# Kernel tuning notes

Measured on AMD Instinct MI355X. Metric: run time of the kernel, lower is better.

The kernel has to match this reference:

```python
import jax, jax.numpy as jnp
import numpy as np

B, T, H, W, C = 8, 16, 64, 64, 16
HID = 64  # hidden_dim of each ConvLSTM cell
K = 3     # kernel size


def _convlstm_step(x, h, c, Wk, b):
    # conv over concat([x, h]) -> 4*HID gate channels (i, f, o, g)
    z = jax.lax.conv_general_dilated(
        jnp.concatenate([x, h], axis=-1), Wk,
        window_strides=(1, 1), padding='SAME',
        dimension_numbers=('NHWC', 'HWIO', 'NHWC')) + b
    i, f, o, g = jnp.split(z, 4, axis=-1)
    c_new = jax.nn.sigmoid(f) * c + jax.nn.sigmoid(i) * jnp.tanh(g)
    h_new = jax.nn.sigmoid(o) * jnp.tanh(c_new)
    return h_new, c_new


def setup_inputs() -> dict:
    key = jax.random.key(0)
    k1, k2, k3 = jax.random.split(key, 3)
    enc_input = jax.random.normal(k1, (B, T, H, W, C), jnp.float32)
    # input cell: in_channels = C + HID; stacked hidden cell: 2*HID
    W0 = jax.random.normal(k2, (K, K, C + HID, 4 * HID), jnp.float32) * 0.05
    b0 = jnp.zeros((4 * HID,), jnp.float32)
    W1 = jax.random.normal(k3, (K, K, 2 * HID, 4 * HID), jnp.float32) * 0.05
    b1 = jnp.zeros((4 * HID,), jnp.float32)
    return {"enc_input": enc_input, "W0": W0, "b0": b0, "W1": W1, "b1": b1}


def reference(enc_input, W0, b0, W1, b1):
    Bv, Tv, Hv, Wv, _ = enc_input.shape
    z0 = jnp.zeros((Bv, Hv, Wv, HID), enc_input.dtype)

    def step(carry, x_t):
        h0, c0, h1, c1 = carry
        h0, c0 = _convlstm_step(x_t, h0, c0, W0, b0)   # input ConvLSTM
        h1, c1 = _convlstm_step(h0, h1, c1, W1, b1)    # stacked hidden ConvLSTM
        return (h0, c0, h1, c1), None

    xs = jnp.moveaxis(enc_input, 1, 0)  # [T, B, H, W, C]
    (h0, c0, h1, c1), _ = jax.lax.scan(step, (z0, z0, z0, z0), xs)
    # Encoder returns last hidden layer's (h, c)
    return (h1, c1)
```

## Files before the change

kernel.cpp:

```cpp
#include <hip/hip_runtime.h>
#include <hip/hip_bf16.h>

#define Bv 8
#define Tv 16
#define Hv 64
#define Wv 64
#define Cv 16
#define HID 64
#define PH 66

typedef short short8 __attribute__((ext_vector_type(8)));
typedef float f32x4 __attribute__((ext_vector_type(4)));
typedef unsigned short u16x8 __attribute__((ext_vector_type(8)));

__device__ __forceinline__ unsigned short f2bf(float x) {
  union { float f; unsigned int u; } v; v.f = x;
  unsigned int r = v.u + 0x7FFF + ((v.u >> 16) & 1);
  return (unsigned short)(r >> 16);
}
__device__ __forceinline__ float sigmoid_f(float x) {
  return 1.f / (1.f + __expf(-x));
}
__device__ __forceinline__ float tanh_f(float x) {
  float e = __expf(2.f * x);
  return 1.f - 2.f / (e + 1.f);
}

__global__ void relayout_w0(const float* __restrict__ W0, unsigned short* __restrict__ out) {
  int o = blockIdx.x * 256 + threadIdx.x;
  if (o >= 27 * 8192) return;
  int cc = o >> 13, t = o & 8191;
  int wn = t >> 11, t2 = t & 2047;
  int g = t2 >> 9, t3 = t2 & 511;
  int l = t3 >> 3, e = t3 & 7;
  int kg = l >> 4, r = l & 15;
  int k = kg * 8 + e;
  int col = g * 64 + wn * 16 + r;
  int tap = cc / 3, cgi = cc - tap * 3;
  int p = cgi * 32 + k;
  float v = 0.f;
  if (p < 16)        v = W0[(size_t)(tap * 80 + p) * 256 + col];
  else if (p >= 32)  v = W0[(size_t)(tap * 80 + (p - 16)) * 256 + col];
  out[o] = f2bf(v);
}
__global__ void relayout_w1(const float* __restrict__ W1, unsigned short* __restrict__ out) {
  int o = blockIdx.x * 256 + threadIdx.x;
  if (o >= 36 * 8192) return;
  int cc = o >> 13, t = o & 8191;
  int wn = t >> 11, t2 = t & 2047;
  int g = t2 >> 9, t3 = t2 & 511;
  int l = t3 >> 3, e = t3 & 7;
  int kg = l >> 4, r = l & 15;
  int k = kg * 8 + e;
  int col = g * 64 + wn * 16 + r;
  int tap = cc >> 2, cgi = cc & 3;
  out[o] = f2bf(W1[(size_t)(tap * 128 + cgi * 32 + k) * 256 + col]);
}

__global__ void zero_init(unsigned short* __restrict__ h0a, unsigned short* __restrict__ h0b,
                          unsigned short* __restrict__ h1a, unsigned short* __restrict__ h1b,
                          unsigned short* __restrict__ xb) {
  int idx = blockIdx.x * 256 + threadIdx.x;
  u16x8 z = {};
  const int XB_CH = (Bv * PH * PH * 32 * 2) / 16;
  if (idx < XB_CH) { *(u16x8*)(xb + idx * 8) = z; return; }
  idx -= XB_CH;
  int bufi = idx / 16640;
  if (bufi >= 4) return;
  int rem = idx - bufi * 16640;
  int b = rem / 2080, r2 = rem - b * 2080;
  int hp = r2 >> 3, c8 = r2 & 7;
  int y, x;
  if (hp < 66)       { y = 0;  x = hp; }
  else if (hp < 132) { y = 65; x = hp - 66; }
  else { int i2 = hp - 132; y = 1 + (i2 >> 1); x = (i2 & 1) * 65; }
  unsigned short* base = (bufi == 0) ? h0a : (bufi == 1) ? h0b : (bufi == 2) ? h1a : h1b;
  *(u16x8*)(base + ((size_t)((b * PH + y) * PH) + x) * 64 + c8 * 8) = z;
}

__global__ void convert_x0(const float* __restrict__ enc, unsigned short* __restrict__ xb) {
  int idx = blockIdx.x * 256 + threadIdx.x;
  int b = idx >> 12, pix = idx & 4095;
  int y = pix >> 6, x = pix & 63;
  const float* s = enc + ((size_t)(b * Tv + 0) * 4096 + pix) * 16;
  float4 f0 = *(const float4*)(s);
  float4 f1 = *(const float4*)(s + 4);
  float4 f2 = *(const float4*)(s + 8);
  float4 f3 = *(const float4*)(s + 12);
  u16x8 o0, o1;
  o0[0]=f2bf(f0.x); o0[1]=f2bf(f0.y); o0[2]=f2bf(f0.z); o0[3]=f2bf(f0.w);
  o0[4]=f2bf(f1.x); o0[5]=f2bf(f1.y); o0[6]=f2bf(f1.z); o0[7]=f2bf(f1.w);
  o1[0]=f2bf(f2.x); o1[1]=f2bf(f2.y); o1[2]=f2bf(f2.z); o1[3]=f2bf(f2.w);
  o1[4]=f2bf(f3.x); o1[5]=f2bf(f3.y); o1[6]=f2bf(f3.z); o1[7]=f2bf(f3.w);
  unsigned short* d = xb + ((size_t)((b * PH + y + 1) * PH) + (x + 1)) * 32;
  *(u16x8*)(d)     = o0;
  *(u16x8*)(d + 8) = o1;
}

template<int CELL, bool T0>
__global__ __launch_bounds__(512, 2)
void cell_mfma(const unsigned short* __restrict__ A0, const unsigned short* __restrict__ A1,
               const unsigned short* __restrict__ Wr, const float* __restrict__ bias,
               float* __restrict__ cbuf, unsigned short* __restrict__ hout,
               float* __restrict__ h1f, float* __restrict__ c1f,
               const float* __restrict__ enc, int tnext, unsigned short* __restrict__ xnext)
{
  constexpr int NC = T0 ? (CELL == 0 ? 9 : 18) : (CELL == 0 ? 27 : 36);
  extern __shared__ char lds[];

  const int tid = threadIdx.x;
  const int l = tid & 63, w = tid >> 6;
  const int wm = w >> 2, wn = w & 3;
  const int gid = blockIdx.x;
  const int bx = gid & 7, by = (gid >> 3) & 3, b = gid >> 5;
  const int r = l & 15, kg = l >> 4;
  const int j = wn * 16 + r;

  const char* bases[2] = {(const char*)A0, (const char*)A1};

  int pixs;
  {
    int ps = w * 16 + r;
    int ys = by * 16 + (ps >> 3), xs = bx * 8 + (ps & 7);
    pixs = (b * PH + ys) * PH + xs;
  }

  float bi[4];
#pragma unroll
  for (int g = 0; g < 4; ++g) bi[g] = bias[g * 64 + j];
  float cpre[4][4] = {};
  if constexpr (!T0) {
#pragma unroll
    for (int mi = 0; mi < 4; ++mi) {
#pragma unroll
      for (int rg = 0; rg < 4; ++rg) {
        int p = wm * 64 + mi * 16 + kg * 4 + rg;
        int y = by * 16 + (p >> 3), x = bx * 8 + (p & 7);
        cpre[mi][rg] = cbuf[((size_t)((b * Hv + y) * Wv) + x) * HID + j];
      }
    }
  }

  auto ISSUE = [&](int cc, int buf) {
    char* dst = lds + buf * 24576;
    int tap, cgi, wcc;
    if (CELL == 0) {
      if (T0) { tap = cc; cgi = 0; wcc = cc * 3; }
      else    { tap = cc / 3; cgi = cc - tap * 3; wcc = cc; }
    } else {
      if (T0) { tap = cc >> 1; cgi = cc & 1; wcc = tap * 4 + cgi; }
      else    { tap = cc >> 2; cgi = cc & 3; wcc = cc; }
    }
    int ky = tap / 3, kx = tap - ky * 3;
    const char* srcb;
    unsigned aoff;
    if (CELL == 0) {
      if (cgi == 0) { srcb = bases[0]; aoff = (unsigned)((pixs + ky * PH + kx) * 64 + kg * 16); }
      else { srcb = bases[1];
             aoff = (unsigned)((pixs + ky * PH + kx) * 128 + ((cgi == 2) ? 64 : 0) + kg * 16); }
    } else {
      srcb = bases[cgi >> 1];
      aoff = (unsigned)((pixs + ky * PH + kx) * 128 + (cgi & 1) * 64 + kg * 16);
    }
    __builtin_amdgcn_global_load_lds((const unsigned int*)(srcb + aoff),
                                     (unsigned int*)(dst + w * 1024), 16, 0, 0);
    const char* wp = (const char*)Wr + (size_t)wcc * 16384 + (unsigned)(w * 2048 + l * 16);
    __builtin_amdgcn_global_load_lds((const unsigned int*)(wp),
                                     (unsigned int*)(dst + 8192 + w * 2048), 16, 0, 0);
    __builtin_amdgcn_global_load_lds((const unsigned int*)(wp + 1024),
                                     (unsigned int*)(dst + 8192 + w * 2048 + 1024), 16, 0, 0);
  };

  f32x4 acc[4][4] = {};
  short8 af[2][4], bfv[2][4];

  ISSUE(0, 0); ISSUE(1, 1); ISSUE(2, 2); ISSUE(3, 3);
#pragma unroll
  for (int cc = 0; cc < NC; ++cc) {
    if (cc <= NC - 4)      { asm volatile("s_waitcnt vmcnt(9)" ::: "memory"); }
    else if (cc == NC - 3) { asm volatile("s_waitcnt vmcnt(6)" ::: "memory"); }
    else if (cc == NC - 2) { asm volatile("s_waitcnt vmcnt(3)" ::: "memory"); }
    else                   { asm volatile("s_waitcnt vmcnt(0)" ::: "memory"); }
    __builtin_amdgcn_sched_barrier(0);
    __builtin_amdgcn_s_barrier();
    __builtin_amdgcn_sched_barrier(0);

    const int q = cc & 1;
    const char* bufp = lds + (cc % 5) * 24576;
#pragma unroll
    for (int mi = 0; mi < 4; ++mi)
      af[q][mi] = *(const short8*)(bufp + (wm * 4 + mi) * 1024 + l * 16);
#pragma unroll
    for (int g = 0; g < 4; ++g)
      bfv[q][g] = *(const short8*)(bufp + 8192 + (wn * 4 + g) * 1024 + l * 16);

    if (cc > 0) {
      asm volatile("s_waitcnt lgkmcnt(8)" ::: "memory");
      __builtin_amdgcn_sched_barrier(0);
    }
    if (cc + 4 < NC) ISSUE(cc + 4, (cc + 4) % 5);
    if (cc > 0) {
      const int qp = q ^ 1;
#pragma unroll
      for (int mi = 0; mi < 4; ++mi)
#pragma unroll
        for (int g = 0; g < 4; ++g)
          acc[mi][g] = __builtin_amdgcn_mfma_f32_16x16x32_bf16(
              af[qp][mi], bfv[qp][g], acc[mi][g], 0, 0, 0);
    }
  }
  asm volatile("s_waitcnt lgkmcnt(0)" ::: "memory");
  __builtin_amdgcn_sched_barrier(0);
  {
    const int qp = (NC - 1) & 1;
#pragma unroll
    for (int mi = 0; mi < 4; ++mi)
#pragma unroll
      for (int g = 0; g < 4; ++g)
        acc[mi][g] = __builtin_amdgcn_mfma_f32_16x16x32_bf16(
            af[qp][mi], bfv[qp][g], acc[mi][g], 0, 0, 0);
  }

#pragma unroll
  for (int mi = 0; mi < 4; ++mi) {
#pragma unroll
    for (int rg = 0; rg < 4; ++rg) {
      int p = wm * 64 + mi * 16 + kg * 4 + rg;
      int y = by * 16 + (p >> 3), x = bx * 8 + (p & 7);
      float zi = acc[mi][0][rg] + bi[0];
      float zf = acc[mi][1][rg] + bi[1];
      float zo = acc[mi][2][rg] + bi[2];
      float zg = acc[mi][3][rg] + bi[3];
      float co = cpre[mi][rg];
      float cn = sigmoid_f(zf) * co + sigmoid_f(zi) * tanh_f(zg);
      float hn = sigmoid_f(zo) * tanh_f(cn);
      size_t ci = ((size_t)((b * Hv + y) * Wv) + x) * HID + j;
      cbuf[ci] = cn;
      hout[((size_t)((b * PH + y + 1) * PH) + (x + 1)) * HID + j] = f2bf(hn);
      if (CELL == 1 && h1f != nullptr) {
        h1f[ci] = hn;
        c1f[ci] = cn;
      }
    }
  }

  if (CELL == 1 && tnext < Tv) {
    int px = gid * 128 + (tid >> 2), q4 = tid & 3;
    int bb = px >> 12, pix = px & 4095;
    int y = pix >> 6, x = pix & 63;
    const float* s = enc + ((size_t)(bb * Tv + tnext) * 4096 + pix) * 16 + q4 * 4;
    float4 f = *(const float4*)s;
    unsigned short* d = xnext + ((size_t)((bb * PH + y + 1) * PH) + (x + 1)) * 32 + q4 * 4;
    d[0] = f2bf(f.x); d[1] = f2bf(f.y); d[2] = f2bf(f.z); d[3] = f2bf(f.w);
  }
}

extern "C" void kernel_launch(void* const* d_in, const int* in_sizes, int n_in,
                              void* d_out, int out_size, void* d_ws, size_t ws_size,
                              hipStream_t stream) {
  const float* enc = (const float*)d_in[0];
  const float* W0  = (const float*)d_in[1];
  const float* b0  = (const float*)d_in[2];
  const float* W1  = (const float*)d_in[3];
  const float* b1  = (const float*)d_in[4];

  float* out = (float*)d_out;
  const size_t NST = (size_t)Bv * Hv * Wv * HID;
  float* h1f = out;
  float* c1  = out + NST;

  char* ws = (char*)d_ws;
  const size_t SZ_C = NST * 4;
  const size_t SZ_H = (size_t)Bv * PH * PH * HID * 2;
  const size_t SZ_X = (size_t)Bv * PH * PH * 32 * 2;
  float*          c0  = (float*)ws;
  unsigned short* h0a = (unsigned short*)(ws + SZ_C);
  unsigned short* h0b = (unsigned short*)(ws + SZ_C + SZ_H);
  unsigned short* h1a = (unsigned short*)(ws + SZ_C + 2 * SZ_H);
  unsigned short* h1b = (unsigned short*)(ws + SZ_C + 3 * SZ_H);
  unsigned short* xb  = (unsigned short*)(ws + SZ_C + 4 * SZ_H);
  unsigned short* w0r = (unsigned short*)(ws + SZ_C + 4 * SZ_H + SZ_X);
  unsigned short* w1r = (unsigned short*)(ws + SZ_C + 4 * SZ_H + SZ_X + (size_t)27 * 16384);

  hipFuncSetAttribute((const void*)cell_mfma<0,false>, hipFuncAttributeMaxDynamicSharedMemorySize, 131072);
  hipFuncSetAttribute((const void*)cell_mfma<0,true>,  hipFuncAttributeMaxDynamicSharedMemorySize, 131072);
  hipFuncSetAttribute((const void*)cell_mfma<1,false>, hipFuncAttributeMaxDynamicSharedMemorySize, 131072);
  hipFuncSetAttribute((const void*)cell_mfma<1,true>,  hipFuncAttributeMaxDynamicSharedMemorySize, 131072);

  zero_init<<<805, 256, 0, stream>>>(h0a, h0b, h1a, h1b, xb);
  relayout_w0<<<864, 256, 0, stream>>>(W0, w0r);
  relayout_w1<<<1152, 256, 0, stream>>>(W1, w1r);
  convert_x0<<<128, 256, 0, stream>>>(enc, xb);

  dim3 grid(256), block(512);
  for (int t = 0; t < Tv; ++t) {
    const bool last = (t == Tv - 1);
    unsigned short* h0r = (t & 1) ? h0b : h0a;
    unsigned short* h0w = (t & 1) ? h0a : h0b;
    unsigned short* h1r = (t & 1) ? h1b : h1a;
    unsigned short* h1w = (t & 1) ? h1a : h1b;
    if (t == 0) {
      cell_mfma<0,true><<<grid, block, 122880, stream>>>(
          xb, h0r, w0r, b0, c0, h0w, nullptr, nullptr, nullptr, Tv, nullptr);
      cell_mfma<1,true><<<grid, block, 122880, stream>>>(
          h0w, h1r, w1r, b1, c1, h1w, nullptr, nullptr, enc, 1, xb);
    } else {
      cell_mfma<0,false><<<grid, block, 122880, stream>>>(
          xb, h0r, w0r, b0, c0, h0w, nullptr, nullptr, nullptr, Tv, nullptr);
      cell_mfma<1,false><<<grid, block, 122880, stream>>>(
          h0w, h1r, w1r, b1, c1, h1w, last ? h1f : nullptr, last ? c1 : nullptr,
          enc, t + 1, xb);
    }
  }
}
```

Baseline: 714.8 us.

## Load weight fragments directly into registers, shrinking the LDS ring to activations only

Weight B-fragments now go straight from global memory into a 4-deep register ring via inline global_load_dwordx4, two chunks ahead, instead of being staged through LDS. The LDS ring now holds only the activation tiles, which cuts dynamic shared memory from 120 KB to 40 KB per block. This could let two blocks share a CU and removes the LDS reads for weights. In exchange it uses more VGPRs and needs hand-computed vmcnt wait counts that must match the order of the mixed loads exactly.

```diff
diff --git a/kernel.cpp b/kernel.cpp
--- a/kernel.cpp
+++ b/kernel.cpp
@@ -24,6 +24,33 @@
 __device__ __forceinline__ float tanh_f(float x) {
   float e = __expf(2.f * x);
   return 1.f - 2.f / (e + 1.f);
+}
+
+__device__ __forceinline__ void waitv_rt(int n) {
+  if      (n <= 0)  asm volatile("s_waitcnt vmcnt(0)" ::: "memory");
+  else if (n == 1)  asm volatile("s_waitcnt vmcnt(1)" ::: "memory");
+  else if (n == 2)  asm volatile("s_waitcnt vmcnt(2)" ::: "memory");
+  else if (n == 3)  asm volatile("s_waitcnt vmcnt(3)" ::: "memory");
+  else if (n == 4)  asm volatile("s_waitcnt vmcnt(4)" ::: "memory");
+  else if (n == 5)  asm volatile("s_waitcnt vmcnt(5)" ::: "memory");
+  else if (n == 6)  asm volatile("s_waitcnt vmcnt(6)" ::: "memory");
+  else if (n == 7)  asm volatile("s_waitcnt vmcnt(7)" ::: "memory");
+  else if (n == 8)  asm volatile("s_waitcnt vmcnt(8)" ::: "memory");
+  else if (n == 9)  asm volatile("s_waitcnt vmcnt(9)" ::: "memory");
+  else if (n == 10) asm volatile("s_waitcnt vmcnt(10)" ::: "memory");
+  else if (n == 11) asm volatile("s_waitcnt vmcnt(11)" ::: "memory");
+  else              asm volatile("s_waitcnt vmcnt(12)" ::: "memory");
+}
+__device__ __forceinline__ constexpr int bS(int i, int NC) {
+  return ((i + 2 <= NC - 1) ? 4 : 0) + ((i + 4 <= NC - 1) ? 1 : 0);
+}
+__device__ __forceinline__ constexpr int NWAIT(int cc, int NC) {
+  if (cc >= NC - 1) return 0;
+  if (cc == 0) return 11;
+  if (cc == 1) return 9;
+  if (cc == 2) return 10;
+  int n = bS(cc - 3, NC) + bS(cc - 2, NC) + bS(cc - 1, NC) - 4;
+  return n < 0 ? 0 : n;
 }
 
 __global__ void relayout_w0(const float* __restrict__ W0, unsigned short* __restrict__ out) {
@@ -141,15 +168,23 @@
     }
   }
 
-  auto ISSUE = [&](int cc, int buf) {
-    char* dst = lds + buf * 24576;
-    int tap, cgi, wcc;
+  const unsigned long long wbase = (unsigned long long)Wr;
+  const unsigned wvo_base = (unsigned)(wn * 4096 + l * 16);
+
+  auto wcc_of = [&](int cc) -> int {
+    if (CELL == 0) return T0 ? cc * 3 : cc;
+    else           return T0 ? ((cc >> 1) * 4 + (cc & 1)) : cc;
+  };
+
+  auto ISSUE_A = [&](int cc, int buf) {
+    char* dst = lds + buf * 8192;
+    int tap, cgi;
     if (CELL == 0) {
-      if (T0) { tap = cc; cgi = 0; wcc = cc * 3; }
-      else    { tap = cc / 3; cgi = cc - tap * 3; wcc = cc; }
+      if (T0) { tap = cc; cgi = 0; }
+      else    { tap = cc / 3; cgi = cc - tap * 3; }
     } else {
-      if (T0) { tap = cc >> 1; cgi = cc & 1; wcc = tap * 4 + cgi; }
-      else    { tap = cc >> 2; cgi = cc & 3; wcc = cc; }
+      if (T0) { tap = cc >> 1; cgi = cc & 1; }
+      else    { tap = cc >> 2; cgi = cc & 3; }
     }
     int ky = tap / 3, kx = tap - ky * 3;
     const char* srcb;
@@ -164,61 +199,75 @@
     }
     __builtin_amdgcn_global_load_lds((const unsigned int*)(srcb + aoff),
                                      (unsigned int*)(dst + w * 1024), 16, 0, 0);
-    const char* wp = (const char*)Wr + (size_t)wcc * 16384 + (unsigned)(w * 2048 + l * 16);
-    __builtin_amdgcn_global_load_lds((const unsigned int*)(wp),
-                                     (unsigned int*)(dst + 8192 + w * 2048), 16, 0, 0);
-    __builtin_amdgcn_global_load_lds((const unsigned int*)(wp + 1024),
-                                     (unsigned int*)(dst + 8192 + w * 2048 + 1024), 16, 0, 0);
   };
 
+  short8 bfv[4][4];
+
+  auto ISSUE_W = [&](int cc) {
+    const int s = cc & 3;
+    unsigned vo = wvo_base + (unsigned)(wcc_of(cc) * 16384);
+    asm volatile("global_load_dwordx4 %0, %1, %2"
+                 : "=&v"(bfv[s][0]) : "v"(vo), "s"(wbase) : "memory");
+    asm volatile("global_load_dwordx4 %0, %1, %2 offset:1024"
+                 : "=&v"(bfv[s][1]) : "v"(vo), "s"(wbase) : "memory");
+    asm volatile("global_load_dwordx4 %0, %1, %2 offset:2048"
+                 : "=&v"(bfv[s][2]) : "v"(vo), "s"(wbase) : "memory");
+    asm volatile("global_load_dwordx4 %0, %1, %2 offset:3072"
+                 : "=&v"(bfv[s][3]) : "v"(vo), "s"(wbase) : "memory");
+  };
+
   f32x4 acc[4][4] = {};
-  short8 af[2][4], bfv[2][4];
-
-  ISSUE(0, 0); ISSUE(1, 1); ISSUE(2, 2); ISSUE(3, 3);
+  short8 af[2][4];
+
+  ISSUE_A(0, 0); __builtin_amdgcn_sched_barrier(0);
+  ISSUE_A(1, 1); __builtin_amdgcn_sched_barrier(0);
+  ISSUE_A(2, 2); __builtin_amdgcn_sched_barrier(0);
+  ISSUE_A(3, 3); __builtin_amdgcn_sched_barrier(0);
+  ISSUE_W(0);    __builtin_amdgcn_sched_barrier(0);
+  ISSUE_W(1);    __builtin_amdgcn_sched_barrier(0);
+
 #pragma unroll
   for (int cc = 0; cc < NC; ++cc) {
-    if (cc <= NC - 4)      { asm volatile("s_waitcnt vmcnt(9)" ::: "memory"); }
-    else if (cc == NC - 3) { asm volatile("s_waitcnt vmcnt(6)" ::: "memory"); }
-    else if (cc == NC - 2) { asm volatile("s_waitcnt vmcnt(3)" ::: "memory"); }
-    else                   { asm volatile("s_waitcnt vmcnt(0)" ::: "memory"); }
+    waitv_rt(NWAIT(cc, NC));
     __builtin_amdgcn_sched_barrier(0);
     __builtin_amdgcn_s_barrier();
     __builtin_amdgcn_sched_barrier(0);
 
     const int q = cc & 1;
-    const char* bufp = lds + (cc % 5) * 24576;
+    const char* bufp = lds + (cc % 5) * 8192;
 #pragma unroll
     for (int mi = 0; mi < 4; ++mi)
       af[q][mi] = *(const short8*)(bufp + (wm * 4 + mi) * 1024 + l * 16);
-#pragma unroll
-    for (int g = 0; g < 4; ++g)
-      bfv[q][g] = *(const short8*)(bufp + 8192 + (wn * 4 + g) * 1024 + l * 16);
 
     if (cc > 0) {
-      asm volatile("s_waitcnt lgkmcnt(8)" ::: "memory");
+      asm volatile("s_waitcnt lgkmcnt(4)" ::: "memory");
       __builtin_amdgcn_sched_barrier(0);
     }
-    if (cc + 4 < NC) ISSUE(cc + 4, (cc + 4) % 5);
+    if (cc + 2 < NC) ISSUE_W(cc + 2);
+    __builtin_amdgcn_sched_barrier(0);
+    if (cc + 4 < NC) ISSUE_A(cc + 4, (cc + 4) % 5);
+    __builtin_amdgcn_sched_barrier(0);
+
     if (cc > 0) {
-      const int qp = q ^ 1;
+      const int qp = (cc - 1) & 1, sp = (cc - 1) & 3;
 #pragma unroll
       for (int mi = 0; mi < 4; ++mi)
 #pragma unroll
         for (int g = 0; g < 4; ++g)
           acc[mi][g] = __builtin_amdgcn_mfma_f32_16x16x32_bf16(
-              af[qp][mi], bfv[qp][g], acc[mi][g], 0, 0, 0);
+              af[qp][mi], bfv[sp][g], acc[mi][g], 0, 0, 0);
     }
   }
   asm volatile("s_waitcnt lgkmcnt(0)" ::: "memory");
   __builtin_amdgcn_sched_barrier(0);
   {
-    const int qp = (NC - 1) & 1;
+    const int qp = (NC - 1) & 1, sp = (NC - 1) & 3;
 #pragma unroll
     for (int mi = 0; mi < 4; ++mi)
 #pragma unroll
       for (int g = 0; g < 4; ++g)
         acc[mi][g] = __builtin_amdgcn_mfma_f32_16x16x32_bf16(
-            af[qp][mi], bfv[qp][g], acc[mi][g], 0, 0, 0);
+            af[qp][mi], bfv[sp][g], acc[mi][g], 0, 0, 0);
   }
 
 #pragma unroll
@@ -282,10 +331,10 @@
   unsigned short* w0r = (unsigned short*)(ws + SZ_C + 4 * SZ_H + SZ_X);
   unsigned short* w1r = (unsigned short*)(ws + SZ_C + 4 * SZ_H + SZ_X + (size_t)27 * 16384);
 
-  hipFuncSetAttribute((const void*)cell_mfma<0,false>, hipFuncAttributeMaxDynamicSharedMemorySize, 131072);
-  hipFuncSetAttribute((const void*)cell_mfma<0,true>,  hipFuncAttributeMaxDynamicSharedMemorySize, 131072);
-  hipFuncSetAttribute((const void*)cell_mfma<1,false>, hipFuncAttributeMaxDynamicSharedMemorySize, 131072);
-  hipFuncSetAttribute((const void*)cell_mfma<1,true>,  hipFuncAttributeMaxDynamicSharedMemorySize, 131072);
+  hipFuncSetAttribute((const void*)cell_mfma<0,false>, hipFuncAttributeMaxDynamicSharedMemorySize, 65536);
+  hipFuncSetAttribute((const void*)cell_mfma<0,true>,  hipFuncAttributeMaxDynamicSharedMemorySize, 65536);
+  hipFuncSetAttribute((const void*)cell_mfma<1,false>, hipFuncAttributeMaxDynamicSharedMemorySize, 65536);
+  hipFuncSetAttribute((const void*)cell_mfma<1,true>,  hipFuncAttributeMaxDynamicSharedMemorySize, 65536);
 
   zero_init<<<805, 256, 0, stream>>>(h0a, h0b, h1a, h1b, xb);
   relayout_w0<<<864, 256, 0, stream>>>(W0, w0r);
@@ -300,14 +349,14 @@
     unsigned short* h1r = (t & 1) ? h1b : h1a;
     unsigned short* h1w = (t & 1) ? h1a : h1b;
     if (t == 0) {
-      cell_mfma<0,true><<<grid, block, 122880, stream>>>(
+      cell_mfma<0,true><<<grid, block, 40960, stream>>>(
           xb, h0r, w0r, b0, c0, h0w, nullptr, nullptr, nullptr, Tv, nullptr);
-      cell_mfma<1,true><<<grid, block, 122880, stream>>>(
+      cell_mfma<1,true><<<grid, block, 40960, stream>>>(
           h0w, h1r, w1r, b1, c1, h1w, nullptr, nullptr, enc, 1, xb);
     } else {
-      cell_mfma<0,false><<<grid, block, 122880, stream>>>(
+      cell_mfma<0,false><<<grid, block, 40960, stream>>>(
           xb, h0r, w0r, b0, c0, h0w, nullptr, nullptr, nullptr, Tv, nullptr);
-      cell_mfma<1,false><<<grid, block, 122880, stream>>>(
+      cell_mfma<1,false><<<grid, block, 40960, stream>>>(
           h0w, h1r, w1r, b1, c1, h1w, last ? h1f : nullptr, last ? c1 : nullptr,
           enc, t + 1, xb);
     }
```

Result: slower. 775.4 us (+8.5%).

## Wavefront-fuse cell0(t) and cell1(t-1) into one launch with smaller tiles

Applied to the files above, without the earlier changes.

Restructures the time loop so that each launch runs cell 0 at step t and cell 1 at step t-1 in the same grid, with blocks interleaved. The two layers no longer need to be serialized per step, and the launch count roughly halves. Each block now covers a 64-pixel tile with 256 threads and a 3-stage LDS ring of about 60KB instead of 128 pixels, 512 threads and 5 stages. The x input buffer is double-buffered so the next frame's conversion can run alongside. The costs are shallower prefetch and more blocks, each loading the full weights.

```diff
diff --git a/kernel.cpp b/kernel.cpp
--- a/kernel.cpp
+++ b/kernel.cpp
@@ -24,6 +24,11 @@
 __device__ __forceinline__ float tanh_f(float x) {
   float e = __expf(2.f * x);
   return 1.f - 2.f / (e + 1.f);
+}
+__device__ __forceinline__ void waitv(int n) {
+  if      (n <= 0) asm volatile("s_waitcnt vmcnt(0)" ::: "memory");
+  else if (n == 5) asm volatile("s_waitcnt vmcnt(5)" ::: "memory");
+  else             asm volatile("s_waitcnt vmcnt(10)" ::: "memory");
 }
 
 __global__ void relayout_w0(const float* __restrict__ W0, unsigned short* __restrict__ out) {
@@ -62,7 +67,7 @@
                           unsigned short* __restrict__ xb) {
   int idx = blockIdx.x * 256 + threadIdx.x;
   u16x8 z = {};
-  const int XB_CH = (Bv * PH * PH * 32 * 2) / 16;
+  const int XB_CH = (Bv * PH * PH * 32 * 2 * 2) / 16;
   if (idx < XB_CH) { *(u16x8*)(xb + idx * 8) = z; return; }
   idx -= XB_CH;
   int bufi = idx / 16640;
@@ -97,31 +102,23 @@
   *(u16x8*)(d + 8) = o1;
 }
 
-template<int CELL, bool T0>
-__global__ __launch_bounds__(512, 2)
-void cell_mfma(const unsigned short* __restrict__ A0, const unsigned short* __restrict__ A1,
-               const unsigned short* __restrict__ Wr, const float* __restrict__ bias,
-               float* __restrict__ cbuf, unsigned short* __restrict__ hout,
-               float* __restrict__ h1f, float* __restrict__ c1f,
-               const float* __restrict__ enc, int tnext, unsigned short* __restrict__ xnext)
+template<int CELL, int NC>
+__device__ __forceinline__ void cell_run(
+    const char* __restrict__ A0, const char* __restrict__ A1,
+    const char* __restrict__ Wr, const float* __restrict__ bias,
+    float* __restrict__ cbuf, unsigned short* __restrict__ hout,
+    float* __restrict__ h1fin, float* __restrict__ c1fin,
+    char* lds, int b, int by, int bx, int tid)
 {
-  constexpr int NC = T0 ? (CELL == 0 ? 9 : 18) : (CELL == 0 ? 27 : 36);
-  extern __shared__ char lds[];
-
-  const int tid = threadIdx.x;
+  constexpr bool T0C = (CELL == 0) ? (NC == 9) : (NC == 18);
   const int l = tid & 63, w = tid >> 6;
-  const int wm = w >> 2, wn = w & 3;
-  const int gid = blockIdx.x;
-  const int bx = gid & 7, by = (gid >> 3) & 3, b = gid >> 5;
   const int r = l & 15, kg = l >> 4;
-  const int j = wn * 16 + r;
-
-  const char* bases[2] = {(const char*)A0, (const char*)A1};
+  const int j = w * 16 + r;
 
   int pixs;
   {
     int ps = w * 16 + r;
-    int ys = by * 16 + (ps >> 3), xs = bx * 8 + (ps & 7);
+    int ys = by * 8 + (ps >> 3), xs = bx * 8 + (ps & 7);
     pixs = (b * PH + ys) * PH + xs;
   }
 
@@ -129,76 +126,75 @@
 #pragma unroll
   for (int g = 0; g < 4; ++g) bi[g] = bias[g * 64 + j];
   float cpre[4][4] = {};
-  if constexpr (!T0) {
+  if constexpr (!T0C) {
 #pragma unroll
     for (int mi = 0; mi < 4; ++mi) {
 #pragma unroll
       for (int rg = 0; rg < 4; ++rg) {
-        int p = wm * 64 + mi * 16 + kg * 4 + rg;
-        int y = by * 16 + (p >> 3), x = bx * 8 + (p & 7);
+        int p = mi * 16 + kg * 4 + rg;
+        int y = by * 8 + (p >> 3), x = bx * 8 + (p & 7);
         cpre[mi][rg] = cbuf[((size_t)((b * Hv + y) * Wv) + x) * HID + j];
       }
     }
   }
 
   auto ISSUE = [&](int cc, int buf) {
-    char* dst = lds + buf * 24576;
+    char* dst = lds + buf * 20480;
     int tap, cgi, wcc;
     if (CELL == 0) {
-      if (T0) { tap = cc; cgi = 0; wcc = cc * 3; }
-      else    { tap = cc / 3; cgi = cc - tap * 3; wcc = cc; }
+      if (T0C) { tap = cc; cgi = 0; wcc = cc * 3; }
+      else     { tap = cc / 3; cgi = cc - tap * 3; wcc = cc; }
     } else {
-      if (T0) { tap = cc >> 1; cgi = cc & 1; wcc = tap * 4 + cgi; }
-      else    { tap = cc >> 2; cgi = cc & 3; wcc = cc; }
+      if (T0C) { tap = cc >> 1; cgi = cc & 1; wcc = tap * 4 + cgi; }
+      else     { tap = cc >> 2; cgi = cc & 3; wcc = cc; }
     }
     int ky = tap / 3, kx = tap - ky * 3;
     const char* srcb;
     unsigned aoff;
     if (CELL == 0) {
-      if (cgi == 0) { srcb = bases[0]; aoff = (unsigned)((pixs + ky * PH + kx) * 64 + kg * 16); }
-      else { srcb = bases[1];
+      if (cgi == 0) { srcb = A0; aoff = (unsigned)((pixs + ky * PH + kx) * 64 + kg * 16); }
+      else { srcb = A1;
              aoff = (unsigned)((pixs + ky * PH + kx) * 128 + ((cgi == 2) ? 64 : 0) + kg * 16); }
     } else {
-      srcb = bases[cgi >> 1];
+      srcb = (cgi < 2) ? A0 : A1;
       aoff = (unsigned)((pixs + ky * PH + kx) * 128 + (cgi & 1) * 64 + kg * 16);
     }
     __builtin_amdgcn_global_load_lds((const unsigned int*)(srcb + aoff),
                                      (unsigned int*)(dst + w * 1024), 16, 0, 0);
-    const char* wp = (const char*)Wr + (size_t)wcc * 16384 + (unsigned)(w * 2048 + l * 16);
-    __builtin_amdgcn_global_load_lds((const unsigned int*)(wp),
-                                     (unsigned int*)(dst + 8192 + w * 2048), 16, 0, 0);
-    __builtin_amdgcn_global_load_lds((const unsigned int*)(wp + 1024),
-                                     (unsigned int*)(dst + 8192 + w * 2048 + 1024), 16, 0, 0);
+    const char* wp = Wr + (size_t)wcc * 16384 + (unsigned)(w * 4096 + l * 16);
+#pragma unroll
+    for (int k = 0; k < 4; ++k)
+      __builtin_amdgcn_global_load_lds((const unsigned int*)(wp + k * 1024),
+                                       (unsigned int*)(dst + 4096 + w * 4096 + k * 1024), 16, 0, 0);
   };
 
   f32x4 acc[4][4] = {};
   short8 af[2][4], bfv[2][4];
 
-  ISSUE(0, 0); ISSUE(1, 1); ISSUE(2, 2); ISSUE(3, 3);
+  ISSUE(0, 0); ISSUE(1, 1);
 #pragma unroll
   for (int cc = 0; cc < NC; ++cc) {
-    if (cc <= NC - 4)      { asm volatile("s_waitcnt vmcnt(9)" ::: "memory"); }
-    else if (cc == NC - 3) { asm volatile("s_waitcnt vmcnt(6)" ::: "memory"); }
-    else if (cc == NC - 2) { asm volatile("s_waitcnt vmcnt(3)" ::: "memory"); }
-    else                   { asm volatile("s_waitcnt vmcnt(0)" ::: "memory"); }
+    waitv(cc <= NC - 2 ? 5 : 0);
     __builtin_amdgcn_sched_barrier(0);
     __builtin_amdgcn_s_barrier();
     __builtin_amdgcn_sched_barrier(0);
 
     const int q = cc & 1;
-    const char* bufp = lds + (cc % 5) * 24576;
+    const char* bufp = lds + (cc % 3) * 20480;
 #pragma unroll
     for (int mi = 0; mi < 4; ++mi)
-      af[q][mi] = *(const short8*)(bufp + (wm * 4 + mi) * 1024 + l * 16);
+      af[q][mi] = *(const short8*)(bufp + mi * 1024 + l * 16);
 #pragma unroll
     for (int g = 0; g < 4; ++g)
-      bfv[q][g] = *(const short8*)(bufp + 8192 + (wn * 4 + g) * 1024 + l * 16);
+      bfv[q][g] = *(const short8*)(bufp + 4096 + w * 4096 + g * 1024 + l * 16);
 
     if (cc > 0) {
       asm volatile("s_waitcnt lgkmcnt(8)" ::: "memory");
       __builtin_amdgcn_sched_barrier(0);
     }
-    if (cc + 4 < NC) ISSUE(cc + 4, (cc + 4) % 5);
+    if (cc + 2 < NC) ISSUE(cc + 2, (cc + 2) % 3);
+    __builtin_amdgcn_sched_barrier(0);
+
     if (cc > 0) {
       const int qp = q ^ 1;
 #pragma unroll
@@ -225,8 +221,8 @@
   for (int mi = 0; mi < 4; ++mi) {
 #pragma unroll
     for (int rg = 0; rg < 4; ++rg) {
-      int p = wm * 64 + mi * 16 + kg * 4 + rg;
-      int y = by * 16 + (p >> 3), x = bx * 8 + (p & 7);
+      int p = mi * 16 + kg * 4 + rg;
+      int y = by * 8 + (p >> 3), x = bx * 8 + (p & 7);
       float zi = acc[mi][0][rg] + bi[0];
       float zf = acc[mi][1][rg] + bi[1];
       float zo = acc[mi][2][rg] + bi[2];
@@ -237,21 +233,54 @@
       size_t ci = ((size_t)((b * Hv + y) * Wv) + x) * HID + j;
       cbuf[ci] = cn;
       hout[((size_t)((b * PH + y + 1) * PH) + (x + 1)) * HID + j] = f2bf(hn);
-      if (CELL == 1 && h1f != nullptr) {
-        h1f[ci] = hn;
-        c1f[ci] = cn;
+      if (CELL == 1 && h1fin != nullptr) {
+        h1fin[ci] = hn;
+        c1fin[ci] = cn;
       }
     }
   }
-
-  if (CELL == 1 && tnext < Tv) {
-    int px = gid * 128 + (tid >> 2), q4 = tid & 3;
-    int bb = px >> 12, pix = px & 4095;
-    int y = pix >> 6, x = pix & 63;
-    const float* s = enc + ((size_t)(bb * Tv + tnext) * 4096 + pix) * 16 + q4 * 4;
-    float4 f = *(const float4*)s;
-    unsigned short* d = xnext + ((size_t)((bb * PH + y + 1) * PH) + (x + 1)) * 32 + q4 * 4;
-    d[0] = f2bf(f.x); d[1] = f2bf(f.y); d[2] = f2bf(f.z); d[3] = f2bf(f.w);
+}
+
+template<int NC1, int NC0, bool LAST>
+__global__ __launch_bounds__(256, 2)
+void step_fused(const unsigned short* __restrict__ xbr, unsigned short* __restrict__ xbw,
+                const unsigned short* __restrict__ h0r, unsigned short* __restrict__ h0w,
+                const unsigned short* __restrict__ h1r, unsigned short* __restrict__ h1w,
+                const unsigned short* __restrict__ w0r, const unsigned short* __restrict__ w1r,
+                const float* __restrict__ b0, const float* __restrict__ b1,
+                float* __restrict__ c0, float* __restrict__ c1,
+                float* __restrict__ h1f, float* __restrict__ c1f,
+                const float* __restrict__ enc, int tnext)
+{
+  extern __shared__ char lds[];
+  const int tid = threadIdx.x;
+  const int gid = blockIdx.x;
+  int isC1, tile;
+  if constexpr (NC1 > 0 && NC0 > 0) { isC1 = gid & 1; tile = gid >> 1; }
+  else if constexpr (NC1 > 0)       { isC1 = 1; tile = gid; }
+  else                              { isC1 = 0; tile = gid; }
+  const int b = tile >> 6, rem = tile & 63;
+  const int by = rem >> 3, bx = rem & 7;
+
+  if constexpr (NC1 > 0) {
+    if (isC1) {
+      cell_run<1, NC1>((const char*)h0r, (const char*)h1r, (const char*)w1r, b1,
+                       c1, h1w, LAST ? h1f : nullptr, LAST ? c1f : nullptr,
+                       lds, b, by, bx, tid);
+      return;
+    }
+  }
+  if constexpr (NC0 > 0) {
+    cell_run<0, NC0>((const char*)xbr, (const char*)h0r, (const char*)w0r, b0,
+                     c0, h0w, nullptr, nullptr, lds, b, by, bx, tid);
+    if (tnext >= 0) {
+      int pp = tid >> 2, q4 = tid & 3;
+      int y = by * 8 + (pp >> 3), x = bx * 8 + (pp & 7);
+      const float* s = enc + ((size_t)(b * Tv + tnext) * 4096 + (y * 64 + x)) * 16 + q4 * 4;
+      float4 f = *(const float4*)s;
+      unsigned short* d = xbw + ((size_t)((b * PH + y + 1) * PH) + (x + 1)) * 32 + q4 * 4;
+      d[0] = f2bf(f.x); d[1] = f2bf(f.y); d[2] = f2bf(f.z); d[3] = f2bf(f.w);
+    }
   }
 }
 
@@ -278,38 +307,43 @@
   unsigned short* h0b = (unsigned short*)(ws + SZ_C + SZ_H);
   unsigned short* h1a = (unsigned short*)(ws + SZ_C + 2 * SZ_H);
   unsigned short* h1b = (unsigned short*)(ws + SZ_C + 3 * SZ_H);
-  unsigned short* xb  = (unsigned short*)(ws + SZ_C + 4 * SZ_H);
-  unsigned short* w0r = (unsigned short*)(ws + SZ_C + 4 * SZ_H + SZ_X);
-  unsigned short* w1r = (unsigned short*)(ws + SZ_C + 4 * SZ_H + SZ_X + (size_t)27 * 16384);
-
-  hipFuncSetAttribute((const void*)cell_mfma<0,false>, hipFuncAttributeMaxDynamicSharedMemorySize, 131072);
-  hipFuncSetAttribute((const void*)cell_mfma<0,true>,  hipFuncAttributeMaxDynamicSharedMemorySize, 131072);
-  hipFuncSetAttribute((const void*)cell_mfma<1,false>, hipFuncAttributeMaxDynamicSharedMemorySize, 131072);
-  hipFuncSetAttribute((const void*)cell_mfma<1,true>,  hipFuncAttributeMaxDynamicSharedMemorySize, 131072);
-
-  zero_init<<<805, 256, 0, stream>>>(h0a, h0b, h1a, h1b, xb);
+  unsigned short* xb0 = (unsigned short*)(ws + SZ_C + 4 * SZ_H);
+  unsigned short* xb1 = (unsigned short*)(ws + SZ_C + 4 * SZ_H + SZ_X);
+  unsigned short* w0r = (unsigned short*)(ws + SZ_C + 4 * SZ_H + 2 * SZ_X);
+  unsigned short* w1r = (unsigned short*)(ws + SZ_C + 4 * SZ_H + 2 * SZ_X + (size_t)27 * 16384);
+
+  hipFuncSetAttribute((const void*)step_fused<0,9,false>,  hipFuncAttributeMaxDynamicSharedMemorySize, 65536);
+  hipFuncSetAttribute((const void*)step_fused<18,27,false>,hipFuncAttributeMaxDynamicSharedMemorySize, 65536);
+  hipFuncSetAttribute((const void*)step_fused<36,27,false>,hipFuncAttributeMaxDynamicSharedMemorySize, 65536);
+  hipFuncSetAttribute((const void*)step_fused<36,0,true>,  hipFuncAttributeMaxDynamicSharedMemorySize, 65536);
+
+  zero_init<<<1349, 256, 0, stream>>>(h0a, h0b, h1a, h1b, xb0);
   relayout_w0<<<864, 256, 0, stream>>>(W0, w0r);
   relayout_w1<<<1152, 256, 0, stream>>>(W1, w1r);
-  convert_x0<<<128, 256, 0, stream>>>(enc, xb);
-
-  dim3 grid(256), block(512);
-  for (int t = 0; t < Tv; ++t) {
-    const bool last = (t == Tv - 1);
-    unsigned short* h0r = (t & 1) ? h0b : h0a;
-    unsigned short* h0w = (t & 1) ? h0a : h0b;
+  convert_x0<<<128, 256, 0, stream>>>(enc, xb0);
+
+  const int LDSB = 61440;
+  step_fused<0,9,false><<<512, 256, LDSB, stream>>>(
+      xb0, xb1, h0b, h0a, h1a, h1b, w0r, w1r, b0, b1, c0, c1,
+      nullptr, nullptr, enc, 1);
+  for (int t = 1; t <= 15; ++t) {
+    unsigned short* h0r = (t & 1) ? h0a : h0b;
+    unsigned short* h0w = (t & 1) ? h0b : h0a;
     unsigned short* h1r = (t & 1) ? h1b : h1a;
     unsigned short* h1w = (t & 1) ? h1a : h1b;
-    if (t == 0) {
-      cell_mfma<0,true><<<grid, block, 122880, stream>>>(
-          xb, h0r, w0r, b0, c0, h0w, nullptr, nullptr, nullptr, Tv, nullptr);
-      cell_mfma<1,true><<<grid, block, 122880, stream>>>(
-          h0w, h1r, w1r, b1, c1, h1w, nullptr, nullptr, enc, 1, xb);
-    } else {
-      cell_mfma<0,false><<<grid, block, 122880, stream>>>(
-          xb, h0r, w0r, b0, c0, h0w, nullptr, nullptr, nullptr, Tv, nullptr);
-      cell_mfma<1,false><<<grid, block, 122880, stream>>>(
-          h0w, h1r, w1r, b1, c1, h1w, last ? h1f : nullptr, last ? c1 : nullptr,
-          enc, t + 1, xb);
-    }
-  }
-}
+    unsigned short* xr  = (t & 1) ? xb1 : xb0;
+    unsigned short* xw  = (t & 1) ? xb0 : xb1;
+    int tn = (t + 1 <= 15) ? (t + 1) : -1;
+    if (t == 1)
+      step_fused<18,27,false><<<1024, 256, LDSB, stream>>>(
+          xr, xw, h0r, h0w, h1r, h1w, w0r, w1r, b0, b1, c0, c1,
+          nullptr, nullptr, enc, tn);
+    else
+      step_fused<36,27,false><<<1024, 256, LDSB, stream>>>(
+          xr, xw, h0r, h0w, h1r, h1w, w0r, w1r, b0, b1, c0, c1,
+          nullptr, nullptr, enc, tn);
+  }
+  step_fused<36,0,true><<<512, 256, LDSB, stream>>>(
+      xb0, xb1, h0b, h0a, h1a, h1b, w0r, w1r, b0, b1, c0, c1,
+      h1f, c1, enc, -1);
+}
```

Measured after the change: 746.6 us. 1.04x slower.
